# Performance work log

Hardware: AMD Instinct MI355X
Metric: run time of the kernel (lower is better)

The kernel has to match this reference:

```python
import jax, jax.numpy as jnp
import numpy as np

# Static config (matches init_kwargs)
DIM, HEADS = 192, 6
PL, LAT, LON = 8, 96, 180
WP, WL, WW = 2, 6, 12          # window size (pressure, lat, lon)
SP, SL, SW = 1, 3, 6           # shift size
N = WP * WL * WW               # tokens per window = 144
NPL, NLAT, NLON = PL // WP, LAT // WL, LON // WW   # 4, 16, 15
NW = NPL * NLAT                # type_of_windows = 64 (lat/pl-dependent bias)
HD = DIM // HEADS              # 32
L = PL * LAT * LON
BIAS_LEN = (2 * WW - 1) * WL * WL * WP * WP   # 3312
EPS = 1e-5


def _position_index():
    # Earth-specific relative position index (Pangu): absolute-position
    # dependence along pressure and latitude, relative along longitude.
    zi = np.arange(WP); zj = -np.arange(WP) * WP
    hi = np.arange(WL); hj = -np.arange(WL) * WL
    w = np.arange(WW)
    c1 = np.stack(np.meshgrid(zi, hi, w, indexing='ij')).reshape(3, -1)
    c2 = np.stack(np.meshgrid(zj, hj, w, indexing='ij')).reshape(3, -1)
    c = (c1[:, :, None] - c2[:, None, :]).transpose(1, 2, 0).copy()
    c[:, :, 2] += WW - 1
    c[:, :, 1] *= 2 * WW - 1
    c[:, :, 0] *= (2 * WW - 1) * WL * WL
    return c.sum(-1)  # (N, N) in [0, BIAS_LEN)


def _attn_mask():
    # Shifted-window mask: lon is periodic on the globe (roll only), so
    # masking is applied along pressure and latitude boundaries only.
    img = np.zeros((1, PL, LAT, LON, 1), np.float32)
    cnt = 0
    for pl in (slice(0, -WP), slice(-WP, -SP), slice(-SP, None)):
        for la in (slice(0, -WL), slice(-WL, -SL), slice(-SL, None)):
            img[:, pl, la, :, :] = cnt
            cnt += 1
    mw = img.reshape(1, NPL, WP, NLAT, WL, NLON, WW, 1)
    mw = mw.transpose(0, 5, 1, 3, 2, 4, 6, 7).reshape(NLON, NW, N)
    am = mw[:, :, None, :] - mw[:, :, :, None]
    return np.where(am != 0, -100.0, 0.0).astype(np.float32)  # (NLON, NW, N, N)


POS_IDX = jnp.asarray(_position_index())
ATTN_MASK = jnp.asarray(_attn_mask())


def layer_norm(x, g, b):
    m = x.mean(-1, keepdims=True)
    v = ((x - m) ** 2).mean(-1, keepdims=True)
    return (x - m) * jax.lax.rsqrt(v + EPS) * g + b


def setup_inputs() -> dict:
    key = jax.random.key(0)
    ks = jax.random.split(key, 10)
    s = 0.02
    return {
        'x': jax.random.normal(ks[0], (1, L, DIM), jnp.float32),
        'norm1_g': jnp.ones((DIM,), jnp.float32),
        'norm1_b': jnp.zeros((DIM,), jnp.float32),
        'qkv_w': jax.random.normal(ks[1], (DIM, 3 * DIM), jnp.float32) * s,
        'qkv_b': jnp.zeros((3 * DIM,), jnp.float32),
        'earth_bias': jax.random.normal(ks[2], (BIAS_LEN, NW, HEADS), jnp.float32) * s,
        'proj_w': jax.random.normal(ks[3], (DIM, DIM), jnp.float32) * s,
        'proj_b': jnp.zeros((DIM,), jnp.float32),
        'norm2_g': jnp.ones((DIM,), jnp.float32),
        'norm2_b': jnp.zeros((DIM,), jnp.float32),
        'fc1_w': jax.random.normal(ks[4], (DIM, 4 * DIM), jnp.float32) * s,
        'fc1_b': jnp.zeros((4 * DIM,), jnp.float32),
        'fc2_w': jax.random.normal(ks[5], (4 * DIM, DIM), jnp.float32) * s,
        'fc2_b': jnp.zeros((DIM,), jnp.float32),
    }


def reference(x, norm1_g, norm1_b, qkv_w, qkv_b, earth_bias, proj_w, proj_b,
              norm2_g, norm2_b, fc1_w, fc1_b, fc2_w, fc2_b):
    B, Ltok, C = x.shape
    shortcut = x
    h = layer_norm(x, norm1_g, norm1_b).reshape(B, PL, LAT, LON, C)
    # shifted windows (lon is periodic -> plain roll)
    h = jnp.roll(h, shift=(-SP, -SL, -SW), axis=(1, 2, 3))
    # window partition -> (B*NLON, NW, N, C); lon windows folded into batch
    xw = h.reshape(B, NPL, WP, NLAT, WL, NLON, WW, C)
    xw = xw.transpose(0, 5, 1, 3, 2, 4, 6, 7).reshape(B * NLON, NW, N, C)
    # earth-specific attention
    qkv = (xw @ qkv_w + qkv_b).reshape(B * NLON, NW, N, 3, HEADS, HD)
    qkv = qkv.transpose(3, 0, 1, 4, 2, 5)  # (3, B_, NW, H, N, HD)
    q, k, v = qkv[0], qkv[1], qkv[2]
    attn = jnp.einsum('bwhnd,bwhmd->bwhnm', q * (HD ** -0.5), k)
    bias = earth_bias[POS_IDX].reshape(N, N, NW, HEADS).transpose(2, 3, 0, 1)
    attn = attn + bias[None]                        # (B_, NW, H, N, N)
    attn = attn.reshape(B, NLON, NW, HEADS, N, N) + ATTN_MASK[None, :, :, None]
    attn = jax.nn.softmax(attn.reshape(B * NLON, NW, HEADS, N, N), axis=-1)
    out = jnp.einsum('bwhnm,bwhmd->bwhnd', attn, v)
    out = out.transpose(0, 1, 3, 2, 4).reshape(B * NLON, NW, N, C)
    out = out @ proj_w + proj_b
    # window reverse + roll back
    h = out.reshape(B, NLON, NPL, NLAT, WP, WL, WW, C)
    h = h.transpose(0, 2, 4, 3, 5, 1, 6, 7).reshape(B, PL, LAT, LON, C)
    h = jnp.roll(h, shift=(SP, SL, SW), axis=(1, 2, 3)).reshape(B, Ltok, C)
    x = shortcut + h
    # MLP block (GELU exact, as nn.GELU default)
    y = layer_norm(x, norm2_g, norm2_b)
    y = jax.nn.gelu(y @ fc1_w + fc1_b, approximate=False) @ fc2_w + fc2_b
    return x + y
```

## Files before the change

### kernel.cpp

```cpp
#include <hip/hip_runtime.h>
#include <hip/hip_bf16.h>
#include <math.h>

typedef unsigned short u16;
typedef __attribute__((ext_vector_type(8))) short short8;
typedef __attribute__((ext_vector_type(4))) short short4v;
typedef __attribute__((ext_vector_type(4))) float f32x4;

#define MFMA(a,b,c) __builtin_amdgcn_mfma_f32_16x16x32_bf16(a,b,c,0,0,0)
#define DIM 192

__device__ __forceinline__ float bf2f(u16 u){ unsigned v=((unsigned)u)<<16; float f; __builtin_memcpy(&f,&v,4); return f; }
__device__ __forceinline__ u16 f2bf(float f){ unsigned v; __builtin_memcpy(&v,&f,4); v = v + 0x7fffu + ((v>>16)&1u); return (u16)(v>>16); }

__device__ __forceinline__ void gl_lds16(const u16* g, u16* l){
  __builtin_amdgcn_global_load_lds((const __attribute__((address_space(1))) unsigned int*)g,
                                   (__attribute__((address_space(3))) unsigned int*)l, 16, 0, 0);
}

__device__ __forceinline__ int win_to_tok(int r){
  int lon = r/9216; int rem = r - lon*9216;
  int w = rem/144, n = rem - w*144;
  int ip=w>>4, il=w&15;
  int wp=n/72, t=n-wp*72, wl=t/12, ww=t-wl*12;
  int p=ip*2+wp, la=il*6+wl, lo=lon*12+ww;
  int p0=p+1;  if(p0>=8)   p0-=8;
  int la0=la+3; if(la0>=96) la0-=96;
  int lo0=lo+6; if(lo0>=180)lo0-=180;
  return (p0*96+la0)*180+lo0;
}

__global__ __launch_bounds__(256) void ln1_window_kernel(
    const float* __restrict__ x, const float* __restrict__ g, const float* __restrict__ b,
    u16* __restrict__ A)
{
  int r = blockIdx.x*4 + (threadIdx.x>>6);
  int lane = threadIdx.x & 63;
  size_t src = (size_t)win_to_tok(r)*DIM;
  float v0=x[src+lane], v1=x[src+64+lane], v2=x[src+128+lane];
  float s=v0+v1+v2;
  for(int m=32;m>=1;m>>=1) s += __shfl_xor(s,m);
  float mean = s*(1.f/192.f);
  float d0=v0-mean,d1=v1-mean,d2=v2-mean;
  float q=d0*d0+d1*d1+d2*d2;
  for(int m=32;m>=1;m>>=1) q += __shfl_xor(q,m);
  float rstd = rsqrtf(q*(1.f/192.f)+1e-5f);
  size_t o = (size_t)r*DIM;
  A[o+lane]     = f2bf(d0*rstd*g[lane]     + b[lane]);
  A[o+64+lane]  = f2bf(d1*rstd*g[64+lane]  + b[64+lane]);
  A[o+128+lane] = f2bf(d2*rstd*g[128+lane] + b[128+lane]);
}

__global__ __launch_bounds__(256) void transpose_bf16_kernel(
    const float* __restrict__ src, u16* __restrict__ dst, int K, int N)
{
  int idx = blockIdx.x*256 + threadIdx.x;
  if (idx >= K*N) return;
  int k = idx / N, n = idx - k*N;
  dst[n*K + k] = f2bf(src[idx]);
}

__global__ __launch_bounds__(256) void pf_w1_kernel(const float* __restrict__ fc1w, u16* __restrict__ W1f){
  int idx = blockIdx.x*256 + threadIdx.x;
  int e = idx & 7, g3 = idx >> 3;
  int g = g3 % 24, r3 = g3 / 24;
  int r = r3 & 31, hc = r3 >> 5;
  int k = ((g ^ (r&7))<<3) + e;
  W1f[idx] = f2bf(fc1w[(size_t)k*768 + hc*32 + r]);
}
__global__ __launch_bounds__(256) void pf_w2_kernel(const float* __restrict__ fc2w, u16* __restrict__ W2f){
  int idx = blockIdx.x*256 + threadIdx.x;
  int e = idx & 7, g3 = idx >> 3;
  int g = g3 & 3, r3 = g3 >> 2;
  int r = r3 % 192, hc = r3 / 192;
  int k = hc*32 + ((g ^ (r&3))<<3) + e;
  W2f[idx] = f2bf(fc2w[(size_t)k*192 + r]);
}

__global__ __launch_bounds__(256) void bias_expand_kernel(
    const float* __restrict__ eb, u16* __restrict__ B2)
{
  __shared__ int t1s[144], t2s[144], rgs[144];
  __shared__ float ebs[3312];
  int bid = blockIdx.x;
  int w = bid / 6;
  int tid = threadIdx.x;
  if (tid < 144) {
    int n = tid;
    int wp=n/72, t=n-wp*72, wl=t/12, ww=t-wl*12;
    t1s[n] = wp*828 + wl*23 + ww;
    t2s[n] = 1656*wp + 138*wl - ww + 11;
    int ip = w>>4, il = w&15;
    int p = ip*2+wp, la = il*6+wl;
    int rp = (p<6)?0:((p<7)?1:2);
    int rl = (la<90)?0:((la<93)?1:2);
    rgs[n] = rp*3+rl;
  }
  for (int i = tid; i < 3312; i += 256) ebs[i] = eb[(size_t)i*384 + bid];
  __syncthreads();
  size_t ob = (size_t)bid*20736;
  for (int idx = tid; idx < 20736; idx += 256) {
    int i = idx & 3, lane = (idx>>2)&63, t = idx>>8;
    int mt = t%9, nt = t/9;
    int n = nt*16 + (lane&15);
    int m = mt*16 + ((lane>>4)<<2) + i;
    float bv = ebs[t1s[n]+t2s[m]];
    bv += (rgs[n]==rgs[m]) ? 0.f : -100.f;
    B2[ob + idx] = f2bf(bv);
  }
}

#define SM_WS   0
#define SM_QS   36864
#define SM_KS   48384
#define SM_VS   59904
#define SM_PS   0
#define SMEM3   70656

__global__ __launch_bounds__(576) void attn_kernel(
    const u16* __restrict__ A,
    const u16* __restrict__ Wt,
    const float* __restrict__ qkvb,
    const u16* __restrict__ Bexp,
    u16* __restrict__ O)
{
  extern __shared__ char smem[];
  u16* Ws = (u16*)(smem + SM_WS);
  u16* qs = (u16*)(smem + SM_QS);
  u16* ks_= (u16*)(smem + SM_KS);
  u16* vs = (u16*)(smem + SM_VS);
  u16* Ps = (u16*)(smem + SM_PS);

  int bid = blockIdx.x;
  int logical = (bid & 7)*720 + (bid >> 3);
  int lon = logical % 15;
  int wh  = logical / 15;
  int h = wh % 6, w = wh / 6;
  int tid = threadIdx.x, lane = tid & 63, wv = tid >> 6;

  {
    int rr = tid % 96, chunk = tid / 96;
    int mat = rr >> 5, c = rr & 31;
    const u16* s = Wt + (size_t)(mat*192 + h*32 + c)*192 + chunk*32;
    uint4 t0 = *(const uint4*)(s);
    uint4 t1 = *(const uint4*)(s+8);
    uint4 t2 = *(const uint4*)(s+16);
    uint4 t3 = *(const uint4*)(s+24);
    u16* d = Ws + rr*192;
    int r7 = rr & 7, g0 = chunk*4;
    *(uint4*)(d + ((g0  )^r7)*8) = t0;
    *(uint4*)(d + ((g0+1)^r7)*8) = t1;
    *(uint4*)(d + ((g0+2)^r7)*8) = t2;
    *(uint4*)(d + ((g0+3)^r7)*8) = t3;
  }
  if (tid < 512) { int c = tid>>4; vs[c*168 + 144 + (tid&15)] = 0; }
  __syncthreads();

  size_t winbase = (size_t)(lon*64 + w)*144;
  int r0 = wv*16;
  int l15 = lane & 15, lg = lane >> 4;
  int sw7 = l15 & 7;

  short8 af[6];
  {
    const u16* arow = A + (winbase + r0 + l15)*DIM + 8*lg;
    #pragma unroll
    for (int k0=0;k0<6;k0++) af[k0] = *(const short8*)(arow + k0*32);
  }
  const float qscale = 0.17677669529663687f;

  #pragma unroll
  for (int mt=0; mt<2; mt++) {
    f32x4 acc = {0.f,0.f,0.f,0.f};
    const u16* wrow = Ws + (mt*16 + l15)*192;
    #pragma unroll
    for (int k0=0;k0<6;k0++) acc = MFMA(*(const short8*)(wrow + ((k0*4+lg)^sw7)*8), af[k0], acc);
    short4v pk;
    #pragma unroll
    for (int i=0;i<4;i++) pk[i] = (short)f2bf((acc[i] + qkvb[h*32 + mt*16 + 4*lg + i])*qscale);
    *(short4v*)(qs + (r0 + l15)*40 + mt*16 + 4*lg) = pk;
  }
  #pragma unroll
  for (int mt=0; mt<2; mt++) {
    f32x4 acc = {0.f,0.f,0.f,0.f};
    const u16* wrow = Ws + (32 + mt*16 + l15)*192;
    #pragma unroll
    for (int k0=0;k0<6;k0++) acc = MFMA(*(const short8*)(wrow + ((k0*4+lg)^sw7)*8), af[k0], acc);
    short4v pk;
    #pragma unroll
    for (int i=0;i<4;i++) pk[i] = (short)f2bf(acc[i] + qkvb[192 + h*32 + mt*16 + 4*lg + i]);
    *(short4v*)(ks_ + (r0 + l15)*40 + mt*16 + 4*lg) = pk;
  }
  #pragma unroll
  for (int ct=0; ct<2; ct++) {
    f32x4 acc = {0.f,0.f,0.f,0.f};
    const u16* wrow = Ws + (64 + ct*16 + l15)*192;
    #pragma unroll
    for (int k0=0;k0<6;k0++) acc = MFMA(af[k0], *(const short8*)(wrow + ((k0*4+lg)^sw7)*8), acc);
    float bias = qkvb[384 + h*32 + ct*16 + l15];
    short4v pk;
    #pragma unroll
    for (int i=0;i<4;i++) pk[i] = (short)f2bf(acc[i] + bias);
    *(short4v*)(vs + (ct*16 + l15)*168 + r0 + 4*lg) = pk;
  }
  __syncthreads();

  short8 bq = *(const short8*)(qs + (r0 + l15)*40 + 8*lg);
  f32x4 sa[9];
  #pragma unroll
  for (int mt=0; mt<9; mt++) {
    f32x4 z = {0.f,0.f,0.f,0.f};
    sa[mt] = MFMA(*(const short8*)(ks_ + (mt*16 + l15)*40 + 8*lg), bq, z);
  }
  __syncthreads();

  {
    const u16* bb = Bexp + (((size_t)wh*9 + wv)*9)*256 + lane*4;
    #pragma unroll
    for (int mt=0; mt<9; mt++) {
      short4v pk = *(const short4v*)(bb + mt*256);
      #pragma unroll
      for (int i=0;i<4;i++) sa[mt][i] += bf2f((u16)pk[i]);
    }
  }
  float rsum = 0.f;
  #pragma unroll
  for (int mt=0; mt<9; mt++)
    #pragma unroll
    for (int i=0;i<4;i++) { float e = __expf(sa[mt][i]); sa[mt][i] = e; rsum += e; }
  rsum += __shfl_xor(rsum, 16);
  rsum += __shfl_xor(rsum, 32);
  float rinv = 1.f / rsum;
  #pragma unroll
  for (int mt=0; mt<9; mt++) {
    short4v pk;
    #pragma unroll
    for (int i=0;i<4;i++) pk[i] = (short)f2bf(sa[mt][i]);
    *(short4v*)(Ps + (r0 + l15)*168 + mt*16 + 4*lg) = pk;
  }
  {
    short4v z = {0,0,0,0};
    *(short4v*)(Ps + (r0 + l15)*168 + 144 + 4*lg) = z;
  }

  #pragma unroll
  for (int ct2=0; ct2<2; ct2++) {
    f32x4 acc = {0.f,0.f,0.f,0.f};
    const u16* vr = vs + (ct2*16 + l15)*168 + 8*lg;
    const u16* pr = Ps + (r0 + l15)*168 + 8*lg;
    #pragma unroll
    for (int k0=0;k0<5;k0++) acc = MFMA(*(const short8*)(vr + 32*k0), *(const short8*)(pr + 32*k0), acc);
    short4v pk;
    #pragma unroll
    for (int i=0;i<4;i++) pk[i] = (short)f2bf(acc[i]*rinv);
    *(short4v*)(O + (winbase + r0 + l15)*DIM + h*32 + ct2*16 + 4*lg) = pk;
  }
}

#define SMEMP (73728 + 512)
__global__ __launch_bounds__(512, 4) void proj_ln2_kernel(
    const u16* __restrict__ AT,
    const u16* __restrict__ Pw,
    const float* __restrict__ pb, const float* __restrict__ x,
    const float* __restrict__ n2g, const float* __restrict__ n2b,
    float* __restrict__ out, u16* __restrict__ Y)
{
  extern __shared__ char smem[];
  u16* Pws = (u16*)smem;
  int* tokmap = (int*)(smem + 73728);
  int tid = threadIdx.x;
  size_t rbase = (size_t)blockIdx.x*128;
  #pragma unroll
  for (int j=0;j<9;j++){
    int g = j*512 + tid;
    int row = g/24, jj = g - row*24;
    uint4 t = *(const uint4*)(Pw + (size_t)row*192 + jj*8);
    *(uint4*)(Pws + row*192 + ((jj ^ (row&7))*8)) = t;
  }
  if (tid < 128) tokmap[tid] = win_to_tok((int)rbase + tid);
  __syncthreads();

  int lane = tid&63, wv = tid>>6, r0 = wv*16;
  int l15 = lane&15, lg = lane>>4;
  short8 af[6];
  const u16* arow = AT + (rbase + r0 + l15)*DIM + 8*lg;
  #pragma unroll
  for (int k0=0;k0<6;k0++) af[k0] = *(const short8*)(arow + k0*32);

  f32x4 acc[12];
  #pragma unroll
  for (int ct=0; ct<12; ct++) {
    f32x4 a = {0.f,0.f,0.f,0.f};
    const u16* wr = Pws + (ct*16+l15)*192;
    #pragma unroll
    for (int k0=0;k0<6;k0++) a = MFMA(af[k0], *(const short8*)(wr + (((k0*4+lg)^(l15&7))*8)), a);
    acc[ct] = a;
  }
  int toks[4];
  #pragma unroll
  for (int i=0;i<4;i++) toks[i] = tokmap[r0 + 4*lg + i];
  #pragma unroll
  for (int ct=0; ct<12; ct++) {
    int col = ct*16+l15;
    float bias = pb[col];
    #pragma unroll
    for (int i=0;i<4;i++){
      size_t o = (size_t)toks[i]*DIM + col;
      float v = x[o] + acc[ct][i] + bias;
      out[o] = v;
      acc[ct][i] = v;
    }
  }
  float s[4] = {0,0,0,0};
  #pragma unroll
  for (int ct=0; ct<12; ct++) for (int i=0;i<4;i++) s[i] += acc[ct][i];
  #pragma unroll
  for (int i=0;i<4;i++){ for (int m=1;m<16;m<<=1) s[i] += __shfl_xor(s[i], m, 16); s[i] *= (1.f/192.f); }
  float q[4] = {0,0,0,0};
  #pragma unroll
  for (int ct=0; ct<12; ct++) for (int i=0;i<4;i++){ float d = acc[ct][i]-s[i]; q[i] += d*d; }
  #pragma unroll
  for (int i=0;i<4;i++){ for (int m=1;m<16;m<<=1) q[i] += __shfl_xor(q[i], m, 16); q[i] = rsqrtf(q[i]*(1.f/192.f)+1e-5f); }
  #pragma unroll
  for (int ct=0; ct<12; ct++) {
    int col = ct*16+l15;
    float gg = n2g[col], bb = n2b[col];
    #pragma unroll
    for (int i=0;i<4;i++)
      Y[(size_t)toks[i]*DIM + col] = f2bf((acc[ct][i]-s[i])*q[i]*gg + bb);
  }
}

#define SMEM5 59392
__global__ __launch_bounds__(512, 4) void mlp_kernel(
    const u16* __restrict__ Y,
    const u16* __restrict__ W1f,
    const float* __restrict__ b1,
    const u16* __restrict__ W2f,
    const float* __restrict__ b2,
    float* __restrict__ out)
{
  extern __shared__ char smem[];
  u16* W1b0 = (u16*)smem;
  u16* W1b1 = (u16*)(smem + 12288);
  u16* W2b0 = (u16*)(smem + 24576);
  u16* W2b1 = (u16*)(smem + 36864);
  u16* Hs   = (u16*)(smem + 49152);
  int tid = threadIdx.x;
  size_t rbase = (size_t)blockIdx.x*128;
  int lane = tid&63, wv = tid>>6, r0 = wv*16;
  int l15 = lane&15, lg = lane>>4;

  short8 af[6];
  {
    const u16* yrow = Y + (rbase + r0 + l15)*DIM + 8*lg;
    #pragma unroll
    for (int k0=0;k0<6;k0++) af[k0] = *(const short8*)(yrow + k0*32);
  }

  {
    gl_lds16(W1f + (size_t)tid*8, W1b0 + tid*8);
    if (tid < 256) gl_lds16(W1f + (size_t)(512+tid)*8, W1b0 + (512+tid)*8);
    gl_lds16(W2f + (size_t)tid*8, W2b0 + tid*8);
    if (tid < 256) gl_lds16(W2f + (size_t)(512+tid)*8, W2b0 + (512+tid)*8);
    const u16* s1 = W1f + 6144; const u16* s2 = W2f + 6144;
    gl_lds16(s1 + (size_t)tid*8, W1b1 + tid*8);
    if (tid < 256) gl_lds16(s1 + (size_t)(512+tid)*8, W1b1 + (512+tid)*8);
    gl_lds16(s2 + (size_t)tid*8, W2b1 + tid*8);
    if (tid < 256) gl_lds16(s2 + (size_t)(512+tid)*8, W2b1 + (512+tid)*8);
  }
  __syncthreads();

  f32x4 acc2[12];
  #pragma unroll
  for (int i=0;i<12;i++) acc2[i] = (f32x4){0.f,0.f,0.f,0.f};

  const float GA = -1.5957691216057307f;
  const float GB = -0.07135481627272283f;

  for (int hc=0; hc<24; hc++) {
    u16* B1w = (hc&1) ? W1b1 : W1b0;
    u16* B2w = (hc&1) ? W2b1 : W2b0;
    #pragma unroll
    for (int ct=0; ct<2; ct++) {
      f32x4 a1 = {0.f,0.f,0.f,0.f};
      const u16* wr = B1w + (ct*16+l15)*192;
      #pragma unroll
      for (int k0=0;k0<6;k0++) a1 = MFMA(af[k0], *(const short8*)(wr + (((k0*4+lg)^(l15&7))*8)), a1);
      float bb = b1[hc*32 + ct*16 + l15];
      #pragma unroll
      for (int i=0;i<4;i++){
        float v = a1[i] + bb;
        float t = v*v;
        float m = fmaf(t, GB, GA);
        float e = __expf(v*m);
        float hgl = v*__builtin_amdgcn_rcpf(1.f + e);
        Hs[(r0 + 4*lg + i)*40 + ct*16 + l15] = f2bf(hgl);
      }
    }
    {
      short8 ah = *(const short8*)(Hs + (r0+l15)*40 + 8*lg);
      #pragma unroll
      for (int ct2=0; ct2<12; ct2++) {
        const u16* wr2 = B2w + (ct2*16+l15)*32 + ((lg ^ (l15&3))*8);
        acc2[ct2] = MFMA(ah, *(const short8*)(wr2), acc2[ct2]);
      }
    }
    __syncthreads();
    if (hc < 22) {
      const u16* s1 = W1f + (size_t)(hc+2)*6144;
      const u16* s2 = W2f + (size_t)(hc+2)*6144;
      u16* d1 = (hc&1) ? W1b1 : W1b0;
      u16* d2 = (hc&1) ? W2b1 : W2b0;
      gl_lds16(s1 + (size_t)tid*8, d1 + tid*8);
      if (tid < 256) gl_lds16(s1 + (size_t)(512+tid)*8, d1 + (512+tid)*8);
      gl_lds16(s2 + (size_t)tid*8, d2 + tid*8);
      if (tid < 256) gl_lds16(s2 + (size_t)(512+tid)*8, d2 + (512+tid)*8);
    }
  }
  #pragma unroll
  for (int ct2=0; ct2<12; ct2++) {
    int col = ct2*16+l15;
    float bb = b2[col];
    #pragma unroll
    for (int i=0;i<4;i++){
      size_t o = (rbase + r0 + 4*lg + i)*DIM + col;
      out[o] = out[o] + acc2[ct2][i] + bb;
    }
  }
}

extern "C" void kernel_launch(void* const* d_in, const int* in_sizes, int n_in,
                              void* d_out, int out_size, void* d_ws, size_t ws_size,
                              hipStream_t stream) {
  const float* x    = (const float*)d_in[0];
  const float* n1g  = (const float*)d_in[1];
  const float* n1b  = (const float*)d_in[2];
  const float* qkvw = (const float*)d_in[3];
  const float* qkvb = (const float*)d_in[4];
  const float* eb   = (const float*)d_in[5];
  const float* projw= (const float*)d_in[6];
  const float* projb= (const float*)d_in[7];
  const float* n2g  = (const float*)d_in[8];
  const float* n2b  = (const float*)d_in[9];
  const float* fc1w = (const float*)d_in[10];
  const float* fc1b = (const float*)d_in[11];
  const float* fc2w = (const float*)d_in[12];
  const float* fc2b = (const float*)d_in[13];
  float* out = (float*)d_out;
  char* ws = (char*)d_ws;

  u16* A   = (u16*)(ws);
  u16* AT  = (u16*)(ws + 53084160);
  u16* Wq  = (u16*)(ws + 106168320);
  u16* Pw  = (u16*)(ws + 106389504);
  u16* W1f = (u16*)(ws + 106463232);
  u16* W2f = (u16*)(ws + 106758144);
  u16* Bexp = (u16*)d_out;

  hipFuncSetAttribute((const void*)attn_kernel,     hipFuncAttributeMaxDynamicSharedMemorySize, SMEM3);
  hipFuncSetAttribute((const void*)proj_ln2_kernel, hipFuncAttributeMaxDynamicSharedMemorySize, SMEMP);
  hipFuncSetAttribute((const void*)mlp_kernel,      hipFuncAttributeMaxDynamicSharedMemorySize, SMEM5);

  transpose_bf16_kernel<<<432, 256, 0, stream>>>(qkvw, Wq, 192, 576);
  transpose_bf16_kernel<<<144, 256, 0, stream>>>(projw, Pw, 192, 192);
  pf_w1_kernel<<<576, 256, 0, stream>>>(fc1w, W1f);
  pf_w2_kernel<<<576, 256, 0, stream>>>(fc2w, W2f);
  bias_expand_kernel<<<384, 256, 0, stream>>>(eb, Bexp);
  ln1_window_kernel<<<34560, 256, 0, stream>>>(x, n1g, n1b, A);
  attn_kernel<<<5760, 576, SMEM3, stream>>>(A, Wq, qkvb, Bexp, AT);
  proj_ln2_kernel<<<1080, 512, SMEMP, stream>>>(AT, Pw, projb, x, n2g, n2b, out, A);
  mlp_kernel<<<1080, 512, SMEM5, stream>>>(A, W1f, fc1b, W2f, fc2b, out);
}
```

Measured before the change: 442.3 us.

## Fuse projection, LayerNorm2 and MLP into a single tail kernel

Merges proj_ln2_kernel and mlp_kernel into one kernel, so the LN2 output stays in LDS and is fed straight into the MLP MFMAs instead of going through a global bf16 buffer. The post-attention residual is stored in bf16 into the AT buffer in window order, and the final output is written once with the scatter to token order. This removes one launch, the Y round trip, and the fp32 read-modify-write of out in the MLP epilogue. In exchange the residual is now rounded to bf16 before being added back, which lowers accuracy, and shared memory is reused across phases, which needs extra barriers.

```diff
diff --git a/kernel.cpp b/kernel.cpp
--- a/kernel.cpp
+++ b/kernel.cpp
@@ -257,83 +257,12 @@
   }
 }
 
-#define SMEMP (73728 + 512)
-__global__ __launch_bounds__(512, 4) void proj_ln2_kernel(
-    const u16* __restrict__ AT,
+#define SMEMF 74240
+__global__ __launch_bounds__(512, 4) void fused_tail_kernel(
+    u16* __restrict__ AT,
     const u16* __restrict__ Pw,
     const float* __restrict__ pb, const float* __restrict__ x,
     const float* __restrict__ n2g, const float* __restrict__ n2b,
-    float* __restrict__ out, u16* __restrict__ Y)
-{
-  extern __shared__ char smem[];
-  u16* Pws = (u16*)smem;
-  int* tokmap = (int*)(smem + 73728);
-  int tid = threadIdx.x;
-  size_t rbase = (size_t)blockIdx.x*128;
-  #pragma unroll
-  for (int j=0;j<9;j++){
-    int g = j*512 + tid;
-    int row = g/24, jj = g - row*24;
-    uint4 t = *(const uint4*)(Pw + (size_t)row*192 + jj*8);
-    *(uint4*)(Pws + row*192 + ((jj ^ (row&7))*8)) = t;
-  }
-  if (tid < 128) tokmap[tid] = win_to_tok((int)rbase + tid);
-  __syncthreads();
-
-  int lane = tid&63, wv = tid>>6, r0 = wv*16;
-  int l15 = lane&15, lg = lane>>4;
-  short8 af[6];
-  const u16* arow = AT + (rbase + r0 + l15)*DIM + 8*lg;
-  #pragma unroll
-  for (int k0=0;k0<6;k0++) af[k0] = *(const short8*)(arow + k0*32);
-
-  f32x4 acc[12];
-  #pragma unroll
-  for (int ct=0; ct<12; ct++) {
-    f32x4 a = {0.f,0.f,0.f,0.f};
-    const u16* wr = Pws + (ct*16+l15)*192;
-    #pragma unroll
-    for (int k0=0;k0<6;k0++) a = MFMA(af[k0], *(const short8*)(wr + (((k0*4+lg)^(l15&7))*8)), a);
-    acc[ct] = a;
-  }
-  int toks[4];
-  #pragma unroll
-  for (int i=0;i<4;i++) toks[i] = tokmap[r0 + 4*lg + i];
-  #pragma unroll
-  for (int ct=0; ct<12; ct++) {
-    int col = ct*16+l15;
-    float bias = pb[col];
-    #pragma unroll
-    for (int i=0;i<4;i++){
-      size_t o = (size_t)toks[i]*DIM + col;
-      float v = x[o] + acc[ct][i] + bias;
-      out[o] = v;
-      acc[ct][i] = v;
-    }
-  }
-  float s[4] = {0,0,0,0};
-  #pragma unroll
-  for (int ct=0; ct<12; ct++) for (int i=0;i<4;i++) s[i] += acc[ct][i];
-  #pragma unroll
-  for (int i=0;i<4;i++){ for (int m=1;m<16;m<<=1) s[i] += __shfl_xor(s[i], m, 16); s[i] *= (1.f/192.f); }
-  float q[4] = {0,0,0,0};
-  #pragma unroll
-  for (int ct=0; ct<12; ct++) for (int i=0;i<4;i++){ float d = acc[ct][i]-s[i]; q[i] += d*d; }
-  #pragma unroll
-  for (int i=0;i<4;i++){ for (int m=1;m<16;m<<=1) q[i] += __shfl_xor(q[i], m, 16); q[i] = rsqrtf(q[i]*(1.f/192.f)+1e-5f); }
-  #pragma unroll
-  for (int ct=0; ct<12; ct++) {
-    int col = ct*16+l15;
-    float gg = n2g[col], bb = n2b[col];
-    #pragma unroll
-    for (int i=0;i<4;i++)
-      Y[(size_t)toks[i]*DIM + col] = f2bf((acc[ct][i]-s[i])*q[i]*gg + bb);
-  }
-}
-
-#define SMEM5 59392
-__global__ __launch_bounds__(512, 4) void mlp_kernel(
-    const u16* __restrict__ Y,
     const u16* __restrict__ W1f,
     const float* __restrict__ b1,
     const u16* __restrict__ W2f,
@@ -341,22 +270,82 @@
     float* __restrict__ out)
 {
   extern __shared__ char smem[];
+  u16* Pws  = (u16*)smem;
+  u16* Ys   = (u16*)smem;
   u16* W1b0 = (u16*)smem;
   u16* W1b1 = (u16*)(smem + 12288);
   u16* W2b0 = (u16*)(smem + 24576);
   u16* W2b1 = (u16*)(smem + 36864);
   u16* Hs   = (u16*)(smem + 49152);
+  int* tokmap = (int*)(smem + 73728);
   int tid = threadIdx.x;
   size_t rbase = (size_t)blockIdx.x*128;
   int lane = tid&63, wv = tid>>6, r0 = wv*16;
   int l15 = lane&15, lg = lane>>4;
 
+  #pragma unroll
+  for (int j=0;j<9;j++){
+    int g = j*512 + tid;
+    int row = g/24, jj = g - row*24;
+    uint4 t = *(const uint4*)(Pw + (size_t)row*192 + jj*8);
+    *(uint4*)(Pws + row*192 + ((jj ^ (row&7))*8)) = t;
+  }
+  if (tid < 128) tokmap[tid] = win_to_tok((int)rbase + tid);
+  __syncthreads();
+
   short8 af[6];
   {
-    const u16* yrow = Y + (rbase + r0 + l15)*DIM + 8*lg;
-    #pragma unroll
-    for (int k0=0;k0<6;k0++) af[k0] = *(const short8*)(yrow + k0*32);
-  }
+    const u16* arow = AT + (rbase + r0 + l15)*DIM + 8*lg;
+    #pragma unroll
+    for (int k0=0;k0<6;k0++) af[k0] = *(const short8*)(arow + k0*32);
+  }
+  f32x4 acc[12];
+  #pragma unroll
+  for (int ct=0; ct<12; ct++) {
+    f32x4 a = {0.f,0.f,0.f,0.f};
+    const u16* wr = Pws + (ct*16+l15)*192;
+    #pragma unroll
+    for (int k0=0;k0<6;k0++) a = MFMA(af[k0], *(const short8*)(wr + (((k0*4+lg)^(l15&7))*8)), a);
+    acc[ct] = a;
+  }
+  int toks[4];
+  #pragma unroll
+  for (int i=0;i<4;i++) toks[i] = tokmap[r0 + 4*lg + i];
+
+  #pragma unroll
+  for (int ct=0; ct<12; ct++) {
+    int col = ct*16+l15;
+    float bias = pb[col];
+    #pragma unroll
+    for (int i=0;i<4;i++){
+      float v = x[(size_t)toks[i]*DIM + col] + acc[ct][i] + bias;
+      acc[ct][i] = v;
+      AT[(rbase + r0 + 4*lg + i)*DIM + col] = f2bf(v);
+    }
+  }
+  float s[4] = {0,0,0,0};
+  #pragma unroll
+  for (int ct=0; ct<12; ct++) for (int i=0;i<4;i++) s[i] += acc[ct][i];
+  #pragma unroll
+  for (int i=0;i<4;i++){ for (int m=1;m<16;m<<=1) s[i] += __shfl_xor(s[i], m, 16); s[i] *= (1.f/192.f); }
+  float q[4] = {0,0,0,0};
+  #pragma unroll
+  for (int ct=0; ct<12; ct++) for (int i=0;i<4;i++){ float d = acc[ct][i]-s[i]; q[i] += d*d; }
+  #pragma unroll
+  for (int i=0;i<4;i++){ for (int m=1;m<16;m<<=1) q[i] += __shfl_xor(q[i], m, 16); q[i] = rsqrtf(q[i]*(1.f/192.f)+1e-5f); }
+
+  __syncthreads();
+  #pragma unroll
+  for (int ct=0; ct<12; ct++) {
+    int col = ct*16+l15;
+    float gg = n2g[col], bb = n2b[col];
+    #pragma unroll
+    for (int i=0;i<4;i++)
+      Ys[(r0 + 4*lg + i)*200 + col] = f2bf((acc[ct][i]-s[i])*q[i]*gg + bb);
+  }
+  #pragma unroll
+  for (int k0=0;k0<6;k0++) af[k0] = *(const short8*)(Ys + (r0+l15)*200 + k0*32 + 8*lg);
+  __syncthreads();
 
   {
     gl_lds16(W1f + (size_t)tid*8, W1b0 + tid*8);
@@ -424,8 +413,8 @@
     float bb = b2[col];
     #pragma unroll
     for (int i=0;i<4;i++){
-      size_t o = (rbase + r0 + 4*lg + i)*DIM + col;
-      out[o] = out[o] + acc2[ct2][i] + bb;
+      float x2v = bf2f(AT[(rbase + r0 + 4*lg + i)*DIM + col]);
+      out[(size_t)toks[i]*DIM + col] = x2v + acc2[ct2][i] + bb;
     }
   }
 }
@@ -458,9 +447,8 @@
   u16* W2f = (u16*)(ws + 106758144);
   u16* Bexp = (u16*)d_out;
 
-  hipFuncSetAttribute((const void*)attn_kernel,     hipFuncAttributeMaxDynamicSharedMemorySize, SMEM3);
-  hipFuncSetAttribute((const void*)proj_ln2_kernel, hipFuncAttributeMaxDynamicSharedMemorySize, SMEMP);
-  hipFuncSetAttribute((const void*)mlp_kernel,      hipFuncAttributeMaxDynamicSharedMemorySize, SMEM5);
+  hipFuncSetAttribute((const void*)attn_kernel,       hipFuncAttributeMaxDynamicSharedMemorySize, SMEM3);
+  hipFuncSetAttribute((const void*)fused_tail_kernel, hipFuncAttributeMaxDynamicSharedMemorySize, SMEMF);
 
   transpose_bf16_kernel<<<432, 256, 0, stream>>>(qkvw, Wq, 192, 576);
   transpose_bf16_kernel<<<144, 256, 0, stream>>>(projw, Pw, 192, 192);
@@ -469,6 +457,6 @@
   bias_expand_kernel<<<384, 256, 0, stream>>>(eb, Bexp);
   ln1_window_kernel<<<34560, 256, 0, stream>>>(x, n1g, n1b, A);
   attn_kernel<<<5760, 576, SMEM3, stream>>>(A, Wq, qkvb, Bexp, AT);
-  proj_ln2_kernel<<<1080, 512, SMEMP, stream>>>(AT, Pw, projb, x, n2g, n2b, out, A);
-  mlp_kernel<<<1080, 512, SMEM5, stream>>>(A, W1f, fc1b, W2f, fc2b, out);
-}
+  fused_tail_kernel<<<1080, 512, SMEMF, stream>>>(AT, Pw, projb, x, n2g, n2b,
+                                                  W1f, fc1b, W2f, fc2b, out);
+}
```

New measurement: 421.7 us. 1.05x faster.
